# Optimization experiments

Measured on AMD Instinct MI355X. Metric: run time of the kernel, lower is better.

The kernel has to match this reference:

```python
import jax, jax.numpy as jnp
import numpy as np

B, C, S, D = 16, 32, 64, 512
DFF, E = 2048, 8


def setup_inputs() -> dict:
    key = jax.random.key(0)
    ks = jax.random.split(key, 16)
    std = 0.02
    return {
        'x': jax.random.normal(ks[0], (B, C, S, D), jnp.float32),
        'baseline': jax.random.normal(ks[1], (B, C, S, D), jnp.float32),
        'attnres': jax.random.normal(ks[2], (B, C, S, D), jnp.float32),
        'shared_w1': jax.random.normal(ks[3], (DFF, D), jnp.float32) * std,
        'shared_b1': jnp.zeros((DFF,), jnp.float32),
        'shared_w2': jax.random.normal(ks[4], (D, DFF), jnp.float32) * std,
        'shared_b2': jnp.zeros((D,), jnp.float32),
        'spa_router_w': jax.random.normal(ks[5], (E, 3 * D), jnp.float32) * std,
        'spa_router_b': jnp.zeros((E,), jnp.float32),
        'spe_router_w': jax.random.normal(ks[6], (E, 3 * D), jnp.float32) * std,
        'spe_router_b': jnp.zeros((E,), jnp.float32),
        'spa_w1': jax.random.normal(ks[7], (E, DFF, D), jnp.float32) * std,
        'spa_b1': jnp.zeros((E, DFF), jnp.float32),
        'spa_w2': jax.random.normal(ks[8], (E, D, DFF), jnp.float32) * std,
        'spa_b2': jnp.zeros((E, D), jnp.float32),
        'spe_w1': jax.random.normal(ks[9], (E, DFF, D), jnp.float32) * std,
        'spe_b1': jnp.zeros((E, DFF), jnp.float32),
        'spe_w2': jax.random.normal(ks[10], (E, D, DFF), jnp.float32) * std,
        'spe_b2': jnp.zeros((E, D), jnp.float32),
    }


def _route(feat, rw, rb):
    # feat [B, 3D] -> top-1 expert index [B] and its softmax gate weight [B]
    logits = feat @ rw.T + rb            # [B, E]
    p = jax.nn.softmax(logits, axis=-1)
    idx = jnp.argmax(logits, axis=-1)    # [B]
    w = jnp.take_along_axis(p, idx[:, None], axis=-1)[:, 0]
    return idx, w


def _specialist(xf, idx, w1, b1, w2, b2):
    # xf [B, T, D]; per-sample gather of expert weights then batched FFN
    W1, B1 = w1[idx], b1[idx]            # [B, DFF, D], [B, DFF]
    W2, B2 = w2[idx], b2[idx]            # [B, D, DFF], [B, D]
    h = jax.nn.gelu(jnp.einsum('btd,bfd->btf', xf, W1) + B1[:, None, :])
    return jnp.einsum('btf,bdf->btd', h, W2) + B2[:, None, :]


def reference(x, baseline, attnres, shared_w1, shared_b1, shared_w2, shared_b2,
              spa_router_w, spa_router_b, spe_router_w, spe_router_b,
              spa_w1, spa_b1, spa_w2, spa_b2, spe_w1, spe_b1, spe_w2, spe_b2):
    b, d = x.shape[0], x.shape[-1]
    xf = x.reshape(b, -1, d)  # [B, T, D]
    # sample-level AttnRes router features: [B, 3*d_model]
    feat = jnp.concatenate([
        baseline.mean(axis=(1, 2)),
        attnres.mean(axis=(1, 2)),
        (attnres - baseline).mean(axis=(1, 2)),
    ], axis=-1)
    spa_idx, spa_w = _route(feat, spa_router_w, spa_router_b)
    spe_idx, spe_w = _route(feat, spe_router_w, spe_router_b)
    # shared dense FFN (dropout=0 eval)
    shared = jax.nn.gelu(xf @ shared_w1.T + shared_b1) @ shared_w2.T + shared_b2
    spa_out = _specialist(xf, spa_idx, spa_w1, spa_b1, spa_w2, spa_b2)
    spe_out = _specialist(xf, spe_idx, spe_w1, spe_b1, spe_w2, spe_b2)
    y = shared + spa_w[:, None, None] * spa_out + spe_w[:, None, None] * spe_out
    return y.reshape(x.shape)
```

## Files before the change

kernel.cpp:

```cpp
#include <hip/hip_runtime.h>
#include <cstdint>
#include <cstddef>

#define DEV __device__ __forceinline__

typedef unsigned short u16;
typedef _Float16 f16x8 __attribute__((ext_vector_type(8)));
typedef float f32x4 __attribute__((ext_vector_type(4)));

static constexpr int NB  = 16;
static constexpr int T   = 2048;
static constexpr int D   = 512;
static constexpr int DFF = 2048;
static constexpr int NE  = 8;
static constexpr int FEAT = 3 * D;

DEV u16 f2h(float f) {
  _Float16 h = (_Float16)f;
  union { _Float16 h; u16 u; } cv; cv.h = h; return cv.u;
}

DEV float gelu_tanh(float x) {
  float u = 0.7978845608028654f * (x + 0.044715f * x * x * x);
  return 0.5f * x * (1.0f + tanhf(u));
}


__global__ void k_part(const float* __restrict__ base, const float* __restrict__ attn,
                       float* __restrict__ part) {
  const int b = blockIdx.x >> 4, ch = blockIdx.x & 15;
  const int d = threadIdx.x;
  const size_t o = ((size_t)b * T + (size_t)ch * 128) * D + d;
  const float* pb = base + o;
  const float* pa = attn + o;
  float sb = 0.f, sa = 0.f;
  for (int r = 0; r < 128; ++r) { sb += pb[(size_t)r * D]; sa += pa[(size_t)r * D]; }
  part[(b * 16 + ch) * D + d] = sb;
  part[NB * 16 * D + (b * 16 + ch) * D + d] = sa;
}

__global__ void k_feat(const float* __restrict__ part, float* __restrict__ feat) {
  const int b = blockIdx.x, d = threadIdx.x;
  float sb = 0.f, sa = 0.f;
  for (int ch = 0; ch < 16; ++ch) {
    sb += part[(b * 16 + ch) * D + d];
    sa += part[NB * 16 * D + (b * 16 + ch) * D + d];
  }
  sb *= (1.0f / 2048.0f); sa *= (1.0f / 2048.0f);
  feat[b * FEAT + d] = sb;
  feat[b * FEAT + D + d] = sa;
  feat[b * FEAT + 2 * D + d] = sa - sb;
}

__global__ void k_route(const float* __restrict__ feat,
                        const float* __restrict__ rw0, const float* __restrict__ rb0,
                        const float* __restrict__ rw1, const float* __restrict__ rb1,
                        int* __restrict__ idx, float* __restrict__ gate) {
  const int r = blockIdx.x >> 4, b = blockIdx.x & 15;
  const float* rw = (r == 0) ? rw0 : rw1;
  const float* rb = (r == 0) ? rb0 : rb1;
  const int l = threadIdx.x;
  float p[8];
#pragma unroll
  for (int e = 0; e < 8; ++e) p[e] = 0.f;
  const float* f = feat + b * FEAT;
  for (int k = l; k < FEAT; k += 64) {
    const float fv = f[k];
#pragma unroll
    for (int e = 0; e < 8; ++e) p[e] += fv * rw[e * FEAT + k];
  }
#pragma unroll
  for (int off = 32; off >= 1; off >>= 1) {
#pragma unroll
    for (int e = 0; e < 8; ++e) p[e] += __shfl_xor(p[e], off);
  }
  if (l == 0) {
    float best = -1e30f; int bi = 0;
    float lg[8];
#pragma unroll
    for (int e = 0; e < 8; ++e) {
      lg[e] = p[e] + rb[e];
      if (lg[e] > best) { best = lg[e]; bi = e; }
    }
    float s = 0.f;
#pragma unroll
    for (int e = 0; e < 8; ++e) s += expf(lg[e] - best);
    idx[r * 16 + b] = bi;
    gate[r * 16 + b] = 1.0f / s;
  }
}

__global__ void k_btot(const float* __restrict__ b2s, const float* __restrict__ b2a,
                       const float* __restrict__ b2e, const int* __restrict__ idx,
                       const float* __restrict__ gate, float* __restrict__ btot) {
  const int b = blockIdx.x, d = threadIdx.x;
  const int ia = idx[b], ie = idx[16 + b];
  const float ga = gate[b], ge = gate[16 + b];
  btot[b * D + d] = b2s[d] + ga * b2a[ia * D + d] + ge * b2e[ie * D + d];
}

__global__ void k_cast(const float* __restrict__ s, u16* __restrict__ d, long n) {
  const long i = ((long)blockIdx.x * blockDim.x + threadIdx.x) * 4;
  if (i >= n) return;
  const float4 v = *(const float4*)(s + i);
  const unsigned int lo = (unsigned int)f2h(v.x) | ((unsigned int)f2h(v.y) << 16);
  const unsigned int hi = (unsigned int)f2h(v.z) | ((unsigned int)f2h(v.w) << 16);
  *(uint2*)(d + i) = make_uint2(lo, hi);
}


DEV void ld_lds16(const void* g, void* l) {
  __builtin_amdgcn_global_load_lds((const __attribute__((address_space(1))) void*)g,
                                   (__attribute__((address_space(3))) void*)l, 16, 0, 0);
}

template <int NKT>
DEV void gemm_core(const u16* __restrict__ Ab, int lda, const u16* __restrict__ Bb, int ldb,
                   u16* As, u16* Bs, f32x4 (&acc)[4][4]) {
  const int tid = threadIdx.x;
  const int lane = tid & 63, wid = tid >> 6;
  const int wr = wid >> 1, wc = wid & 1;
  const int arow = wr * 64 + (lane & 15);
  const int brow = wc * 64 + (lane & 15);
  const int koff = (lane >> 4) * 8;
  const int srow = tid >> 3;
  const int scol = (tid & 7) * 8;
  const u16* ga = Ab + (size_t)srow * lda + scol;
  const u16* gb = Bb + (size_t)srow * ldb + scol;
  u16* lA = As + wid * 512;
  u16* lB = Bs + wid * 512;

  for (int kt = 0; kt < NKT; ++kt) {
    const int k0 = kt * 64;
#pragma unroll
    for (int i = 0; i < 4; ++i)
      ld_lds16(ga + (size_t)(i * 32) * lda + k0, lA + i * 2048);
#pragma unroll
    for (int i = 0; i < 4; ++i)
      ld_lds16(gb + (size_t)(i * 32) * ldb + k0, lB + i * 2048);
    __syncthreads();
#pragma unroll
    for (int kk = 0; kk < 2; ++kk) {
      f16x8 av[4], bv[4];
#pragma unroll
      for (int m = 0; m < 4; ++m)
        av[m] = *(const f16x8*)(As + (arow + m * 16) * 64 + kk * 32 + koff);
#pragma unroll
      for (int n = 0; n < 4; ++n)
        bv[n] = *(const f16x8*)(Bs + (brow + n * 16) * 64 + kk * 32 + koff);
#pragma unroll
      for (int m = 0; m < 4; ++m) {
#pragma unroll
        for (int n = 0; n < 4; ++n)
          acc[m][n] = __builtin_amdgcn_mfma_f32_16x16x32_f16(av[m], bv[n], acc[m][n], 0, 0, 0);
      }
    }
    __syncthreads();
  }
}

template <int BANK>
__global__ __launch_bounds__(256, 2) void k_ffn1(
    const u16* __restrict__ xh, const u16* __restrict__ w1, const float* __restrict__ b1,
    const int* __restrict__ idx, const float* __restrict__ gate, u16* __restrict__ h) {
  __shared__ alignas(16) u16 As[128 * 64];
  __shared__ alignas(16) u16 Bs[128 * 64];
  const int b = blockIdx.y;
  const int mt = blockIdx.x >> 4;
  const int nt = blockIdx.x & 15;
  const int e = (BANK == 0) ? 0 : idx[(BANK - 1) * 16 + b];
  const float g = (BANK == 0) ? 1.0f : gate[(BANK - 1) * 16 + b];
  const u16* Ab = xh + ((size_t)b * T + (size_t)mt * 128) * D;
  const u16* Bb = w1 + (size_t)e * DFF * D + (size_t)nt * 128 * D;
  const float* bb = b1 + (size_t)e * DFF;

  f32x4 acc[4][4];
#pragma unroll
  for (int m = 0; m < 4; ++m)
#pragma unroll
    for (int n = 0; n < 4; ++n)
#pragma unroll
      for (int r = 0; r < 4; ++r) acc[m][n][r] = 0.f;

  gemm_core<8>(Ab, D, Bb, D, As, Bs, acc);

  const int lane = threadIdx.x & 63, wid = threadIdx.x >> 6;
  const int wr = wid >> 1, wc = wid & 1;
  const int rr = (lane >> 4) << 2, cc = lane & 15;
  u16* hb = h + (size_t)b * T * DFF;
#pragma unroll
  for (int mi = 0; mi < 4; ++mi) {
    const int row = mt * 128 + wr * 64 + mi * 16 + rr;
#pragma unroll
    for (int ni = 0; ni < 4; ++ni) {
      const int col = nt * 128 + wc * 64 + ni * 16 + cc;
      const float bv = bb[col];
      const f32x4 a = acc[mi][ni];
#pragma unroll
      for (int r = 0; r < 4; ++r) {
        const float v = gelu_tanh(a[r] + bv) * g;
        hb[(size_t)(row + r) * DFF + col] = f2h(v);
      }
    }
  }
}

template <int BANK>
__global__ __launch_bounds__(256, 2) void k_ffn2(
    const u16* __restrict__ h, const u16* __restrict__ w2, const float* __restrict__ btot,
    const int* __restrict__ idx, float* __restrict__ out) {
  __shared__ alignas(16) u16 As[128 * 64];
  __shared__ alignas(16) u16 Bs[128 * 64];
  const int b = blockIdx.y;
  const int mt = blockIdx.x >> 2;
  const int nt = blockIdx.x & 3;
  const int e = (BANK == 0) ? 0 : idx[(BANK - 1) * 16 + b];
  const u16* Ab = h + ((size_t)b * T + (size_t)mt * 128) * DFF;
  const u16* Bb = w2 + (size_t)e * D * DFF + (size_t)nt * 128 * DFF;

  f32x4 acc[4][4];
#pragma unroll
  for (int m = 0; m < 4; ++m)
#pragma unroll
    for (int n = 0; n < 4; ++n)
#pragma unroll
      for (int r = 0; r < 4; ++r) acc[m][n][r] = 0.f;

  gemm_core<32>(Ab, DFF, Bb, DFF, As, Bs, acc);

  const int lane = threadIdx.x & 63, wid = threadIdx.x >> 6;
  const int wr = wid >> 1, wc = wid & 1;
  const int rr = (lane >> 4) << 2, cc = lane & 15;
  float* ob = out + (size_t)b * T * D;
  const float* bt = btot + b * D;
#pragma unroll
  for (int mi = 0; mi < 4; ++mi) {
    const int row = mt * 128 + wr * 64 + mi * 16 + rr;
#pragma unroll
    for (int ni = 0; ni < 4; ++ni) {
      const int col = nt * 128 + wc * 64 + ni * 16 + cc;
      const f32x4 a = acc[mi][ni];
#pragma unroll
      for (int r = 0; r < 4; ++r) {
        const size_t oi = (size_t)(row + r) * D + col;
        if (BANK == 0) ob[oi] = a[r] + bt[col];
        else           ob[oi] += a[r];
      }
    }
  }
}


extern "C" void kernel_launch(void* const* d_in, const int* in_sizes, int n_in,
                              void* d_out, int out_size, void* d_ws, size_t ws_size,
                              hipStream_t stream) {
  (void)in_sizes; (void)n_in; (void)out_size; (void)ws_size;
  const float* x    = (const float*)d_in[0];
  const float* base = (const float*)d_in[1];
  const float* attn = (const float*)d_in[2];
  const float* sw1  = (const float*)d_in[3];
  const float* sb1  = (const float*)d_in[4];
  const float* sw2  = (const float*)d_in[5];
  const float* sb2  = (const float*)d_in[6];
  const float* arw  = (const float*)d_in[7];
  const float* arb  = (const float*)d_in[8];
  const float* erw  = (const float*)d_in[9];
  const float* erb  = (const float*)d_in[10];
  const float* aw1  = (const float*)d_in[11];
  const float* ab1  = (const float*)d_in[12];
  const float* aw2  = (const float*)d_in[13];
  const float* ab2  = (const float*)d_in[14];
  const float* ew1  = (const float*)d_in[15];
  const float* eb1  = (const float*)d_in[16];
  const float* ew2  = (const float*)d_in[17];
  const float* eb2  = (const float*)d_in[18];
  float* out = (float*)d_out;

  char* w = (char*)d_ws;
  u16* xh   = (u16*)w;  w += (size_t)NB * T * D * 2;
  u16* hbuf = (u16*)w;  w += (size_t)NB * T * DFF * 2;
  u16* w1s  = (u16*)w;  w += (size_t)DFF * D * 2;
  u16* w2s  = (u16*)w;  w += (size_t)D * DFF * 2;
  u16* w1a  = (u16*)w;  w += (size_t)NE * DFF * D * 2;
  u16* w2a  = (u16*)w;  w += (size_t)NE * D * DFF * 2;
  u16* w1e  = (u16*)w;  w += (size_t)NE * DFF * D * 2;
  u16* w2e  = (u16*)w;  w += (size_t)NE * D * DFF * 2;
  float* part = (float*)w; w += (size_t)2 * NB * 16 * D * 4;
  float* feat = (float*)w; w += (size_t)NB * FEAT * 4;
  int*   idx  = (int*)w;   w += 32 * 4;
  float* gate = (float*)w; w += 32 * 4;
  float* btot = (float*)w; w += (size_t)NB * D * 4;

  k_part<<<dim3(256), dim3(512), 0, stream>>>(base, attn, part);
  k_feat<<<dim3(16), dim3(512), 0, stream>>>(part, feat);
  k_route<<<dim3(32), dim3(64), 0, stream>>>(feat, arw, arb, erw, erb, idx, gate);
  k_btot<<<dim3(16), dim3(512), 0, stream>>>(sb2, ab2, eb2, idx, gate, btot);

  {
    long n;
    n = (long)NB * T * D;      k_cast<<<(unsigned)(n / 1024), 256, 0, stream>>>(x,   xh,  n);
    n = (long)DFF * D;         k_cast<<<(unsigned)(n / 1024), 256, 0, stream>>>(sw1, w1s, n);
    n = (long)D * DFF;         k_cast<<<(unsigned)(n / 1024), 256, 0, stream>>>(sw2, w2s, n);
    n = (long)NE * DFF * D;    k_cast<<<(unsigned)(n / 1024), 256, 0, stream>>>(aw1, w1a, n);
    n = (long)NE * D * DFF;    k_cast<<<(unsigned)(n / 1024), 256, 0, stream>>>(aw2, w2a, n);
    n = (long)NE * DFF * D;    k_cast<<<(unsigned)(n / 1024), 256, 0, stream>>>(ew1, w1e, n);
    n = (long)NE * D * DFF;    k_cast<<<(unsigned)(n / 1024), 256, 0, stream>>>(ew2, w2e, n);
  }

  const dim3 g1(256, 16), g2(64, 16), blk(256);
  k_ffn1<0><<<g1, blk, 0, stream>>>(xh, w1s, sb1, idx, gate, hbuf);
  k_ffn2<0><<<g2, blk, 0, stream>>>(hbuf, w2s, btot, idx, out);
  k_ffn1<1><<<g1, blk, 0, stream>>>(xh, w1a, ab1, idx, gate, hbuf);
  k_ffn2<1><<<g2, blk, 0, stream>>>(hbuf, w2a, btot, idx, out);
  k_ffn1<2><<<g1, blk, 0, stream>>>(xh, w1e, eb1, idx, gate, hbuf);
  k_ffn2<2><<<g2, blk, 0, stream>>>(hbuf, w2e, btot, idx, out);
}
```

Baseline: 790.1 us.

## Rewrite FFN GEMMs with 256x256 tiles, 4-stage LDS pipeline, swizzle, fast GELU

Replaces the single-buffered 128x128 GEMM core with a 256x256 tile, 8-wave core that keeps four stages of 32-wide K chunks in LDS. Global-to-LDS loads are issued several chunks ahead and split across the two MFMA halves, with setprio around the MFMA blocks. LDS uses an XOR swizzle to avoid bank conflicts, and block indices are remapped so blocks that share data run close together. The tanh GELU is replaced by an exp-based sigmoid form with a fast divide. This trades more LDS and registers per block, and slightly different GELU numerics, for less load latency exposure and more data reuse.

```diff
diff --git a/kernel.cpp b/kernel.cpp
--- a/kernel.cpp
+++ b/kernel.cpp
@@ -15,14 +15,17 @@
 static constexpr int NE  = 8;
 static constexpr int FEAT = 3 * D;
 
+#define MFMA16 __builtin_amdgcn_mfma_f32_16x16x32_f16
+
 DEV u16 f2h(float f) {
   _Float16 h = (_Float16)f;
   union { _Float16 h; u16 u; } cv; cv.h = h; return cv.u;
 }
 
-DEV float gelu_tanh(float x) {
-  float u = 0.7978845608028654f * (x + 0.044715f * x * x * x);
-  return 0.5f * x * (1.0f + tanhf(u));
+DEV float gelu_fast(float x) {
+  const float t = x * x;
+  const float p = x * fmaf(t, -0.07135481627f, -1.59576912161f);
+  return __fdividef(x, 1.0f + __expf(p));
 }
 
 
@@ -114,91 +117,151 @@
                                    (__attribute__((address_space(3))) void*)l, 16, 0, 0);
 }
 
-template <int NKT>
-DEV void gemm_core(const u16* __restrict__ Ab, int lda, const u16* __restrict__ Bb, int ldb,
-                   u16* As, u16* Bs, f32x4 (&acc)[4][4]) {
+template <int NC>
+DEV void gemm_pipe(const u16* __restrict__ A, int lda, const u16* __restrict__ B, int ldb,
+                   u16* As, u16* Bs, f32x4 (&acc)[8][4]) {
+  static_assert(NC >= 4, "pipeline needs >=4 chunks");
   const int tid = threadIdx.x;
   const int lane = tid & 63, wid = tid >> 6;
-  const int wr = wid >> 1, wc = wid & 1;
-  const int arow = wr * 64 + (lane & 15);
-  const int brow = wc * 64 + (lane & 15);
-  const int koff = (lane >> 4) * 8;
-  const int srow = tid >> 3;
-  const int scol = (tid & 7) * 8;
-  const u16* ga = Ab + (size_t)srow * lda + scol;
-  const u16* gb = Bb + (size_t)srow * ldb + scol;
-  u16* lA = As + wid * 512;
-  u16* lB = Bs + wid * 512;
-
-  for (int kt = 0; kt < NKT; ++kt) {
-    const int k0 = kt * 64;
-#pragma unroll
-    for (int i = 0; i < 4; ++i)
-      ld_lds16(ga + (size_t)(i * 32) * lda + k0, lA + i * 2048);
-#pragma unroll
-    for (int i = 0; i < 4; ++i)
-      ld_lds16(gb + (size_t)(i * 32) * ldb + k0, lB + i * 2048);
-    __syncthreads();
-#pragma unroll
-    for (int kk = 0; kk < 2; ++kk) {
-      f16x8 av[4], bv[4];
-#pragma unroll
-      for (int m = 0; m < 4; ++m)
-        av[m] = *(const f16x8*)(As + (arow + m * 16) * 64 + kk * 32 + koff);
-#pragma unroll
-      for (int n = 0; n < 4; ++n)
-        bv[n] = *(const f16x8*)(Bs + (brow + n * 16) * 64 + kk * 32 + koff);
-#pragma unroll
-      for (int m = 0; m < 4; ++m) {
-#pragma unroll
-        for (int n = 0; n < 4; ++n)
-          acc[m][n] = __builtin_amdgcn_mfma_f32_16x16x32_f16(av[m], bv[n], acc[m][n], 0, 0, 0);
-      }
-    }
-    __syncthreads();
+  const int wr = wid >> 2, wc = wid & 3;
+
+  const int r0 = wid * 32 + (lane >> 2);
+  const int r1 = r0 + 16;
+  const int cb0 = (lane & 3) ^ ((r0 >> 1) & 3);
+  const int cb1 = (lane & 3) ^ ((r1 >> 1) & 3);
+  const int ldsO0 = wid * 1024;
+  const int ldsO1 = wid * 1024 + 512;
+  const u16* gA0 = A + (size_t)r0 * lda + cb0 * 8;
+  const u16* gA1 = A + (size_t)r1 * lda + cb1 * 8;
+  const u16* gB0 = B + (size_t)r0 * ldb + cb0 * 8;
+  const u16* gB1 = B + (size_t)r1 * ldb + cb1 * 8;
+
+  const int kb = lane >> 4;
+  int ar[8], br[4];
+#pragma unroll
+  for (int m = 0; m < 8; ++m) {
+    const int R = wr * 128 + m * 16 + (lane & 15);
+    ar[m] = R * 64 + ((kb ^ ((R >> 1) & 3)) * 16);
+  }
+#pragma unroll
+  for (int n = 0; n < 4; ++n) {
+    const int C = wc * 64 + n * 16 + (lane & 15);
+    br[n] = C * 64 + ((kb ^ ((C >> 1) & 3)) * 16);
+  }
+
+  {
+    const u16 *a0 = gA0, *a1 = gA1, *b0 = gB0, *b1 = gB1;
+#pragma unroll
+    for (int c = 0; c < 3; ++c) {
+      ld_lds16(a0, As + c * 8192 + ldsO0);
+      ld_lds16(a1, As + c * 8192 + ldsO1);
+      ld_lds16(b0, Bs + c * 8192 + ldsO0);
+      ld_lds16(b1, Bs + c * 8192 + ldsO1);
+      a0 += 32; a1 += 32; b0 += 32; b1 += 32;
+    }
+  }
+  const u16 *sA0 = gA0 + 96, *sA1 = gA1 + 96, *sB0 = gB0 + 96, *sB1 = gB1 + 96;
+  asm volatile("s_waitcnt vmcnt(8)" ::: "memory");
+  __builtin_amdgcn_s_barrier();
+
+  for (int ch = 0; ch < NC; ++ch) {
+    const char* Asl = (const char*)(As + (ch & 3) * 8192);
+    const char* Bsl = (const char*)(Bs + (ch & 3) * 8192);
+    const bool st = (ch + 3) < NC;
+    const int ssl = (ch + 3) & 3;
+
+    f16x8 av[8], bv0, bv1, bv2, bv3;
+#pragma unroll
+    for (int m = 0; m < 8; ++m) av[m] = *(const f16x8*)(Asl + ar[m]);
+    bv0 = *(const f16x8*)(Bsl + br[0]);
+    bv1 = *(const f16x8*)(Bsl + br[1]);
+    if (st) {
+      ld_lds16(sA0, As + ssl * 8192 + ldsO0);
+      ld_lds16(sA1, As + ssl * 8192 + ldsO1);
+    }
+    __builtin_amdgcn_s_barrier();
+    asm volatile("s_waitcnt lgkmcnt(0)" ::: "memory");
+    __builtin_amdgcn_s_setprio(1);
+#pragma unroll
+    for (int m = 0; m < 8; ++m) {
+      acc[m][0] = MFMA16(av[m], bv0, acc[m][0], 0, 0, 0);
+      acc[m][1] = MFMA16(av[m], bv1, acc[m][1], 0, 0, 0);
+    }
+    __builtin_amdgcn_s_setprio(0);
+    __builtin_amdgcn_s_barrier();
+
+    bv2 = *(const f16x8*)(Bsl + br[2]);
+    bv3 = *(const f16x8*)(Bsl + br[3]);
+    if (st) {
+      ld_lds16(sB0, Bs + ssl * 8192 + ldsO0);
+      ld_lds16(sB1, Bs + ssl * 8192 + ldsO1);
+    }
+    __builtin_amdgcn_s_barrier();
+    asm volatile("s_waitcnt lgkmcnt(0)" ::: "memory");
+    __builtin_amdgcn_s_setprio(1);
+#pragma unroll
+    for (int m = 0; m < 8; ++m) {
+      acc[m][2] = MFMA16(av[m], bv2, acc[m][2], 0, 0, 0);
+      acc[m][3] = MFMA16(av[m], bv3, acc[m][3], 0, 0, 0);
+    }
+    __builtin_amdgcn_s_setprio(0);
+    sA0 += 32; sA1 += 32; sB0 += 32; sB1 += 32;
+
+    if (ch < NC - 3)       asm volatile("s_waitcnt vmcnt(8)" ::: "memory");
+    else if (ch == NC - 3) asm volatile("s_waitcnt vmcnt(4)" ::: "memory");
+    else if (ch == NC - 2) asm volatile("s_waitcnt vmcnt(0)" ::: "memory");
+    __builtin_amdgcn_s_barrier();
   }
 }
 
 template <int BANK>
-__global__ __launch_bounds__(256, 2) void k_ffn1(
+__global__ __launch_bounds__(512, 2) void k_ffn1(
     const u16* __restrict__ xh, const u16* __restrict__ w1, const float* __restrict__ b1,
     const int* __restrict__ idx, const float* __restrict__ gate, u16* __restrict__ h) {
-  __shared__ alignas(16) u16 As[128 * 64];
-  __shared__ alignas(16) u16 Bs[128 * 64];
-  const int b = blockIdx.y;
-  const int mt = blockIdx.x >> 4;
-  const int nt = blockIdx.x & 15;
-  const int e = (BANK == 0) ? 0 : idx[(BANK - 1) * 16 + b];
+  __shared__ alignas(16) u16 As[4 * 8192];
+  __shared__ alignas(16) u16 Bs[4 * 8192];
+  int wg = blockIdx.x;
+  const int q = (int)gridDim.x >> 3;
+  wg = (wg & 7) * q + (wg >> 3);
+  const int b  = wg >> 6;
+  const int mt = (wg >> 3) & 7;
+  const int nt = wg & 7;
+
+  const int e   = (BANK == 0) ? 0 : idx[(BANK - 1) * 16 + b];
   const float g = (BANK == 0) ? 1.0f : gate[(BANK - 1) * 16 + b];
-  const u16* Ab = xh + ((size_t)b * T + (size_t)mt * 128) * D;
-  const u16* Bb = w1 + (size_t)e * DFF * D + (size_t)nt * 128 * D;
+  const u16* Ab = xh + ((size_t)b * T + (size_t)mt * 256) * D;
+  const u16* Bb = w1 + (size_t)e * DFF * D + (size_t)nt * 256 * D;
   const float* bb = b1 + (size_t)e * DFF;
 
-  f32x4 acc[4][4];
-#pragma unroll
-  for (int m = 0; m < 4; ++m)
+  f32x4 acc[8][4];
+#pragma unroll
+  for (int m = 0; m < 8; ++m)
 #pragma unroll
     for (int n = 0; n < 4; ++n)
 #pragma unroll
       for (int r = 0; r < 4; ++r) acc[m][n][r] = 0.f;
 
-  gemm_core<8>(Ab, D, Bb, D, As, Bs, acc);
+  gemm_pipe<16>(Ab, D, Bb, D, As, Bs, acc);
 
   const int lane = threadIdx.x & 63, wid = threadIdx.x >> 6;
-  const int wr = wid >> 1, wc = wid & 1;
+  const int wr = wid >> 2, wc = wid & 3;
   const int rr = (lane >> 4) << 2, cc = lane & 15;
+  const int mrow = mt * 256 + wr * 128;
+  const int ncol = nt * 256 + wc * 64;
   u16* hb = h + (size_t)b * T * DFF;
-#pragma unroll
-  for (int mi = 0; mi < 4; ++mi) {
-    const int row = mt * 128 + wr * 64 + mi * 16 + rr;
-#pragma unroll
-    for (int ni = 0; ni < 4; ++ni) {
-      const int col = nt * 128 + wc * 64 + ni * 16 + cc;
-      const float bv = bb[col];
-      const f32x4 a = acc[mi][ni];
+  float bias[4];
+#pragma unroll
+  for (int n = 0; n < 4; ++n) bias[n] = bb[ncol + n * 16 + cc];
+#pragma unroll
+  for (int m = 0; m < 8; ++m) {
+    const int row = mrow + m * 16 + rr;
+#pragma unroll
+    for (int n = 0; n < 4; ++n) {
+      const int col = ncol + n * 16 + cc;
+      const f32x4 a = acc[m][n];
 #pragma unroll
       for (int r = 0; r < 4; ++r) {
-        const float v = gelu_tanh(a[r] + bv) * g;
+        const float v = gelu_fast(a[r] + bias[n]) * g;
         hb[(size_t)(row + r) * DFF + col] = f2h(v);
       }
     }
@@ -206,44 +269,52 @@
 }
 
 template <int BANK>
-__global__ __launch_bounds__(256, 2) void k_ffn2(
+__global__ __launch_bounds__(512, 2) void k_ffn2(
     const u16* __restrict__ h, const u16* __restrict__ w2, const float* __restrict__ btot,
     const int* __restrict__ idx, float* __restrict__ out) {
-  __shared__ alignas(16) u16 As[128 * 64];
-  __shared__ alignas(16) u16 Bs[128 * 64];
-  const int b = blockIdx.y;
-  const int mt = blockIdx.x >> 2;
-  const int nt = blockIdx.x & 3;
+  __shared__ alignas(16) u16 As[4 * 8192];
+  __shared__ alignas(16) u16 Bs[4 * 8192];
+  int wg = blockIdx.x;
+  const int q = (int)gridDim.x >> 3;
+  wg = (wg & 7) * q + (wg >> 3);
+  const int b  = wg >> 4;
+  const int mt = (wg >> 1) & 7;
+  const int nt = wg & 1;
+
   const int e = (BANK == 0) ? 0 : idx[(BANK - 1) * 16 + b];
-  const u16* Ab = h + ((size_t)b * T + (size_t)mt * 128) * DFF;
-  const u16* Bb = w2 + (size_t)e * D * DFF + (size_t)nt * 128 * DFF;
-
-  f32x4 acc[4][4];
-#pragma unroll
-  for (int m = 0; m < 4; ++m)
+  const u16* Ab = h + ((size_t)b * T + (size_t)mt * 256) * DFF;
+  const u16* Bb = w2 + (size_t)e * D * DFF + (size_t)nt * 256 * DFF;
+
+  f32x4 acc[8][4];
+#pragma unroll
+  for (int m = 0; m < 8; ++m)
 #pragma unroll
     for (int n = 0; n < 4; ++n)
 #pragma unroll
       for (int r = 0; r < 4; ++r) acc[m][n][r] = 0.f;
 
-  gemm_core<32>(Ab, DFF, Bb, DFF, As, Bs, acc);
+  gemm_pipe<64>(Ab, DFF, Bb, DFF, As, Bs, acc);
 
   const int lane = threadIdx.x & 63, wid = threadIdx.x >> 6;
-  const int wr = wid >> 1, wc = wid & 1;
+  const int wr = wid >> 2, wc = wid & 3;
   const int rr = (lane >> 4) << 2, cc = lane & 15;
+  const int mrow = mt * 256 + wr * 128;
+  const int ncol = nt * 256 + wc * 64;
   float* ob = out + (size_t)b * T * D;
-  const float* bt = btot + b * D;
-#pragma unroll
-  for (int mi = 0; mi < 4; ++mi) {
-    const int row = mt * 128 + wr * 64 + mi * 16 + rr;
-#pragma unroll
-    for (int ni = 0; ni < 4; ++ni) {
-      const int col = nt * 128 + wc * 64 + ni * 16 + cc;
-      const f32x4 a = acc[mi][ni];
+  float bt[4];
+#pragma unroll
+  for (int n = 0; n < 4; ++n) bt[n] = btot[b * D + ncol + n * 16 + cc];
+#pragma unroll
+  for (int m = 0; m < 8; ++m) {
+    const int row = mrow + m * 16 + rr;
+#pragma unroll
+    for (int n = 0; n < 4; ++n) {
+      const int col = ncol + n * 16 + cc;
+      const f32x4 a = acc[m][n];
 #pragma unroll
       for (int r = 0; r < 4; ++r) {
         const size_t oi = (size_t)(row + r) * D + col;
-        if (BANK == 0) ob[oi] = a[r] + bt[col];
+        if (BANK == 0) ob[oi] = a[r] + bt[n];
         else           ob[oi] += a[r];
       }
     }
@@ -307,7 +378,7 @@
     n = (long)NE * D * DFF;    k_cast<<<(unsigned)(n / 1024), 256, 0, stream>>>(ew2, w2e, n);
   }
 
-  const dim3 g1(256, 16), g2(64, 16), blk(256);
+  const dim3 g1(1024), g2(256), blk(512);
   k_ffn1<0><<<g1, blk, 0, stream>>>(xh, w1s, sb1, idx, gate, hbuf);
   k_ffn2<0><<<g2, blk, 0, stream>>>(hbuf, w2s, btot, idx, out);
   k_ffn1<1><<<g1, blk, 0, stream>>>(xh, w1a, ab1, idx, gate, hbuf);
```

New measurement: 737.1 us. -6.7%, faster.
